# Optimization experiments

Measured on AMD Instinct MI355X. Metric: run time of the kernel, lower is better.

Reference implementation:

```python
import jax, jax.numpy as jnp
import numpy as np

DIM = 512
H = 8
HD = DIM // H
MAX_DIST = 128
TABLE = (2 * MAX_DIST + 1) ** 2
LAMBDA_INIT = 0.8


def setup_inputs() -> dict:
    key = jax.random.key(0)
    ks = jax.random.split(key, 20)
    B, Nq, Nkv = 4, 1024, 1024
    inp = {
        "x_q": jax.random.normal(ks[0], (B, Nq, DIM), jnp.float32),
        "x_kv": jax.random.normal(ks[1], (B, Nkv, DIM), jnp.float32),
        "coords_q": jax.random.randint(ks[2], (B, Nq, 2), 0, 256, jnp.int32),
        "coords_k": jax.random.randint(ks[3], (B, Nkv, 2), 0, 256, jnp.int32),
        "alpha_map": jax.random.uniform(ks[4], (B, Nq, 1), jnp.float32),
        "Wq": jax.random.normal(ks[5], (DIM, DIM), jnp.float32) * 0.02,
        "bq": jnp.zeros((DIM,), jnp.float32),
        "Wk": jax.random.normal(ks[6], (DIM, DIM), jnp.float32) * 0.02,
        "bk": jnp.zeros((DIM,), jnp.float32),
        "Wv": jax.random.normal(ks[7], (DIM, DIM), jnp.float32) * 0.02,
        "bv": jnp.zeros((DIM,), jnp.float32),
        "lambda_q1": jax.random.normal(ks[8], (H // 2, HD), jnp.float32) * 0.1,
        "lambda_k1": jax.random.normal(ks[9], (H // 2, HD), jnp.float32) * 0.1,
        "lambda_q2": jax.random.normal(ks[10], (H // 2, HD), jnp.float32) * 0.1,
        "lambda_k2": jax.random.normal(ks[11], (H // 2, HD), jnp.float32) * 0.1,
        "rpe_table": jax.random.normal(ks[12], (TABLE, H), jnp.float32) * 0.02,
        "Wp": jax.random.normal(ks[13], (DIM, DIM), jnp.float32) * 0.02,
        "bp": jnp.zeros((DIM,), jnp.float32),
    }
    return inp


def reference(x_q, x_kv, coords_q, coords_k, alpha_map,
              Wq, bq, Wk, bk, Wv, bv,
              lambda_q1, lambda_k1, lambda_q2, lambda_k2,
              rpe_table, Wp, bp):
    B, Nq, C = x_q.shape
    Nkv = x_kv.shape[1]
    n_half = H // 2
    scale = HD ** -0.5

    # projections -> [B, H, N, HD]
    q = (x_q @ Wq.T + bq).reshape(B, Nq, H, HD).transpose(0, 2, 1, 3)
    k = (x_kv @ Wk.T + bk).reshape(B, Nkv, H, HD).transpose(0, 2, 1, 3)
    v = (x_kv @ Wv.T + bv).reshape(B, Nkv, H, HD).transpose(0, 2, 1, 3)

    # sparse relative position bias: gather per-pair from table
    rel = coords_q[:, :, None, :] - coords_k[:, None, :, :] + MAX_DIST  # [B,Nq,Nkv,2]
    rel = jnp.clip(rel, 0, 2 * MAX_DIST)
    idx = rel[..., 0] * (2 * MAX_DIST + 1) + rel[..., 1]  # [B,Nq,Nkv]
    bias = rpe_table[idx].transpose(0, 3, 1, 2)  # [B,H,Nq,Nkv]

    scores = jnp.einsum('bhqd,bhkd->bhqk', q, k) * scale + bias
    probs = jax.nn.softmax(scores, axis=-1)
    x_std = jnp.einsum('bhqk,bhkd->bhqd', probs, v)

    lam1 = jnp.exp(jnp.sum(lambda_q1 * lambda_k1, axis=-1))  # [n_half]
    lam2 = jnp.exp(jnp.sum(lambda_q2 * lambda_k2, axis=-1))
    lam = (lam1 - lam2 + LAMBDA_INIT)[None, :, None, None]

    attn_diff = probs[:, :n_half] - lam * probs[:, n_half:]
    x_diff = jnp.einsum('bhqk,bhkd->bhqd', attn_diff, v[:, :n_half])

    alpha = alpha_map[:, None]  # [B,1,Nq,1]
    x1 = x_std[:, :n_half] + alpha * x_diff
    x = jnp.concatenate([x1, x_std[:, n_half:]], axis=1)  # [B,H,Nq,HD]
    x = x.transpose(0, 2, 1, 3).reshape(B, Nq, C)
    return x @ Wp.T + bp
```

## Files before the change

### kernel.cpp

```cpp
#include <hip/hip_runtime.h>
#include <cstddef>
#include <cstdint>

#define DIM   512
#define NSEQ  1024
#define NB    4
#define LOG2E 1.44269504f

typedef unsigned short u16;
typedef short bf16x8 __attribute__((ext_vector_type(8)));
typedef _Float16 half8v __attribute__((ext_vector_type(8)));
typedef float f32x4  __attribute__((ext_vector_type(4)));

#define MFMA(a, b, c)  __builtin_amdgcn_mfma_f32_16x16x32_bf16(a, b, c, 0, 0, 0)
#define MFMAH(a, b, c) __builtin_amdgcn_mfma_f32_16x16x32_f16(a, b, c, 0, 0, 0)

__device__ inline void split2(float x, u16& h, u16& l) {
  unsigned u = __float_as_uint(x);
  unsigned hb = (u + 0x7fffu + ((u >> 16) & 1u)) >> 16;
  float fh = __uint_as_float(hb << 16);
  float r = x - fh;
  unsigned v = __float_as_uint(r);
  unsigned lb = (v + 0x7fffu + ((v >> 16) & 1u)) >> 16;
  h = (u16)hb; l = (u16)lb;
}

__device__ inline uint2 pack4(const u16 a[4]) {
  return make_uint2((unsigned)a[0] | ((unsigned)a[1] << 16),
                    (unsigned)a[2] | ((unsigned)a[3] << 16));
}

__device__ inline u16 f2h(float x) {
  _Float16 h = (_Float16)x;
  u16 r; __builtin_memcpy(&r, &h, 2);
  return r;
}
__device__ inline float h2f(u16 b) {
  _Float16 h; __builtin_memcpy(&h, &b, 2);
  return (float)h;
}
__device__ inline unsigned pkh2(float a, float b) {
  return (unsigned)f2h(a) | ((unsigned)f2h(b) << 16);
}

__device__ inline void split_body(const float* __restrict__ in,
                                  u16* __restrict__ out, int e4) {
  const int e = e4 * 4;
  const int m = e >> 9, c = e & 511;
  const float4 v = *(const float4*)(in + e);
  u16 h[4], l[4];
  split2(v.x, h[0], l[0]); split2(v.y, h[1], l[1]);
  split2(v.z, h[2], l[2]); split2(v.w, h[3], l[3]);
  u16* o = out + (size_t)m * 1024 + c;
  *(uint2*)o = pack4(h);
  *(uint2*)(o + 512) = pack4(l);
}

#define GLDS(g, l)                                                        \
  __builtin_amdgcn_global_load_lds(                                       \
      (const __attribute__((address_space(1))) void*)(g),                 \
      (__attribute__((address_space(3))) void*)(l), 16, 0, 0)

__global__ __launch_bounds__(256) void prep(
    const float* __restrict__ wq, const float* __restrict__ wk,
    const float* __restrict__ wv, const float* __restrict__ wp,
    const float* __restrict__ xq, const float* __restrict__ xkv,
    const int* __restrict__ cq, const int* __restrict__ ck,
    const float* __restrict__ rpe,
    u16* __restrict__ w2, u16* __restrict__ xq2, u16* __restrict__ xkv2,
    u16* __restrict__ biasT) {
  __shared__ u16 Ts[8 * 16 * 64];
  const int id = blockIdx.x;
  const int t = threadIdx.x;
  if (id < 1024) {
    const int y = id >> 8;
    const float* src = (y == 0) ? wq : (y == 1) ? wk : (y == 2) ? wv : wp;
    split_body(src, w2 + (size_t)y * 524288, (id & 255) * 256 + t);
  } else if (id < 5120) {
    const int e = id - 1024;
    const int y = e >> 11;
    split_body(y ? xkv : xq, y ? xkv2 : xq2, (e & 2047) * 256 + t);
  } else {
    const int e = id - 5120;
    const int q0 = (e & 15) * 64, k0 = ((e >> 4) & 63) * 16, b = e >> 10;
    const int qn = t & 63, kb = t >> 6;
    const int2 cqv = ((const int2*)cq)[b * NSEQ + q0 + qn];
#pragma unroll
    for (int j = 0; j < 4; ++j) {
      const int k = kb * 4 + j;
      const int2 ckv = ((const int2*)ck)[b * NSEQ + k0 + k];
      const int r0 = min(max(cqv.x - ckv.x + 128, 0), 256);
      const int r1 = min(max(cqv.y - ckv.y + 128, 0), 256);
      const float* rp = rpe + (size_t)(r0 * 257 + r1) * 8;
      const float4 f0 = *(const float4*)rp;
      const float4 f1 = *(const float4*)(rp + 4);
      u16* dst = Ts + k * 64 + qn;
      dst[0 * 1024] = f2h(f0.x * LOG2E); dst[1 * 1024] = f2h(f0.y * LOG2E);
      dst[2 * 1024] = f2h(f0.z * LOG2E); dst[3 * 1024] = f2h(f0.w * LOG2E);
      dst[4 * 1024] = f2h(f1.x * LOG2E); dst[5 * 1024] = f2h(f1.y * LOG2E);
      dst[6 * 1024] = f2h(f1.z * LOG2E); dst[7 * 1024] = f2h(f1.w * LOG2E);
    }
    __syncthreads();
#pragma unroll
    for (int i = 0; i < 4; ++i) {
      const int e2 = i * 256 + t;
      const int row = e2 >> 3, c8 = e2 & 7;
      const int hh = row >> 4, k = row & 15;
      const uint4 v = *(const uint4*)(Ts + row * 64 + c8 * 8);
      *(uint4*)(biasT + ((size_t)(b * 8 + hh) * 1024 + k0 + k) * 1024 +
                q0 + c8 * 8) = v;
    }
  }
}

template <int OUT_MODE>
__device__ __forceinline__ void gemm_db(
    u16 (*__restrict__ As)[8192], u16 (*__restrict__ Bs)[8192],
    const u16* __restrict__ A2, const u16* __restrict__ B2,
    const float* __restrict__ bias, void* __restrict__ outp,
    float scale, int m0, int n0) {
  const int tid = threadIdx.x;
  const int lane = tid & 63, w = tid >> 6;
  const int wm = (w & 1) * 64, wn = (w >> 1) * 64;
  const int lr8 = lane >> 3;
  const int scc = (lane & 7) ^ lr8;
  const int colA = ((scc & 3) * 8) + ((scc >> 2) * 512);

  const int fr = lane & 15, kq = lane >> 4, fx = fr & 7;
  int aoh[4], aol[4], boh[4], bol[4];
#pragma unroll
  for (int i = 0; i < 4; ++i) {
    const int ra = (wm + i * 16 + fr) * 64;
    aoh[i] = ra + ((kq ^ fx)) * 8;
    aol[i] = ra + (((4 + kq) ^ fx)) * 8;
    const int rb = (wn + i * 16 + fr) * 64;
    boh[i] = rb + ((kq ^ fx)) * 8;
    bol[i] = rb + (((4 + kq) ^ fx)) * 8;
  }

  auto stage = [&](int it, int p) {
    const int k0 = it * 32;
#pragma unroll
    for (int i = 0; i < 4; ++i) {
      const int rA = m0 + w * 32 + i * 8 + lr8;
      GLDS(A2 + (size_t)rA * 1024 + colA + k0,
           (char*)As[p] + (w * 32 + i * 8) * 128);
      const int rB = n0 + w * 32 + i * 8 + lr8;
      GLDS(B2 + (size_t)rB * 1024 + colA + k0,
           (char*)Bs[p] + (w * 32 + i * 8) * 128);
    }
  };

  f32x4 acc[4][4] = {};
  stage(0, 0);
  for (int it = 0; it < 16; ++it) {
    const int p = it & 1;
    __syncthreads();
    if (it + 1 < 16) stage(it + 1, p ^ 1);
    const u16* Ab = As[p];
    const u16* Bb = Bs[p];
    bf16x8 ah[4], al[4], bh[4], bl[4];
#pragma unroll
    for (int i = 0; i < 4; ++i) {
      ah[i] = *(const bf16x8*)(Ab + aoh[i]);
      al[i] = *(const bf16x8*)(Ab + aol[i]);
      bh[i] = *(const bf16x8*)(Bb + boh[i]);
      bl[i] = *(const bf16x8*)(Bb + bol[i]);
    }
#pragma unroll
    for (int i = 0; i < 4; ++i)
#pragma unroll
      for (int j = 0; j < 4; ++j) {
        acc[i][j] = MFMA(al[i], bh[j], acc[i][j]);
        acc[i][j] = MFMA(ah[i], bl[j], acc[i][j]);
        acc[i][j] = MFMA(ah[i], bh[j], acc[i][j]);
      }
  }

  const int er = (lane >> 4) * 4, ec = lane & 15;
#pragma unroll
  for (int i = 0; i < 4; ++i)
#pragma unroll
    for (int j = 0; j < 4; ++j) {
      const int row = m0 + wm + i * 16 + er;
      const int col = n0 + wn + j * 16 + ec;
      const float bv = bias[col];
      if (OUT_MODE == 4) {
        u16 hf[4];
#pragma unroll
        for (int r = 0; r < 4; ++r) hf[r] = f2h((acc[i][j][r] + bv) * scale);
        const int bb = row >> 10, kk = row & 1023;
        *(uint2*)((u16*)outp + ((size_t)(bb * 512 + col)) * 1024 + kk) =
            pack4(hf);
      } else {
#pragma unroll
        for (int r = 0; r < 4; ++r) {
          const float v = (acc[i][j][r] + bv) * scale;
          if (OUT_MODE == 3)
            ((u16*)outp)[(size_t)(row + r) * 512 + col] = f2h(v);
          else
            ((float*)outp)[(size_t)(row + r) * 512 + col] = v;
        }
      }
    }
}

__global__ __launch_bounds__(256, 2) void gemm_qkv(
    const u16* __restrict__ xq2, const u16* __restrict__ xkv2,
    const u16* __restrict__ w2, const float* __restrict__ bq,
    const float* __restrict__ bk, const float* __restrict__ bv,
    u16* __restrict__ q2f, u16* __restrict__ k2f, u16* __restrict__ vtf) {
  __shared__ __align__(16) u16 As[2][8192], Bs[2][8192];
  const int z = blockIdx.z;
  const int m0 = blockIdx.x * 128, n0 = blockIdx.y * 128;
  if (z == 0)
    gemm_db<3>(As, Bs, xq2, w2, bq, q2f, 0.125f * LOG2E, m0, n0);
  else if (z == 1)
    gemm_db<3>(As, Bs, xkv2, w2 + 524288, bk, k2f, 1.0f, m0, n0);
  else
    gemm_db<4>(As, Bs, xkv2, w2 + 2 * 524288, bv, vtf, 1.0f, m0, n0);
}

__global__ __launch_bounds__(256, 2) void gemm_out(
    const u16* __restrict__ xa2, const u16* __restrict__ w2p,
    const float* __restrict__ bp, float* __restrict__ out) {
  __shared__ __align__(16) u16 As[2][8192], Bs[2][8192];
  gemm_db<0>(As, Bs, xa2, w2p, bp, out, 1.0f,
             blockIdx.x * 128, blockIdx.y * 128);
}

__global__ __launch_bounds__(512) void attn_f16(
    const u16* __restrict__ q2f, const u16* __restrict__ k2f,
    const u16* __restrict__ vtf, const float* __restrict__ amap,
    const float* __restrict__ lq1, const float* __restrict__ lk1,
    const float* __restrict__ lq2, const float* __restrict__ lk2,
    const u16* __restrict__ biasT, u16* __restrict__ xo) {
  __shared__ __align__(16) u16 KsL[2][2][4096];
  __shared__ __align__(16) u16 VtL[2][2][4096];
  __shared__ float2 mls[2][2][2][16];
  __shared__ float l2s[32];
  __shared__ float lam_s;

  const int tid = threadIdx.x;
  const int lane = tid & 63, w = tid >> 6;
  const int kg = w >> 2, h = (w >> 1) & 1, qs = w & 1;
  const int wl = w & 3;
  const int hp = blockIdx.y, b = blockIdx.z;
  const int q0 = blockIdx.x * 32;
  const int head = hp + 4 * h;
  const int lq = lane & 15, lg = lane >> 4;
  const int q = qs * 16 + lq;
  const size_t qrow = (size_t)(b * NSEQ + q0 + q);

  if (tid < 64) {
    float p1 = lq1[hp * 64 + tid] * lk1[hp * 64 + tid];
    float p2 = lq2[hp * 64 + tid] * lk2[hp * 64 + tid];
#pragma unroll
    for (int m = 32; m >= 1; m >>= 1) {
      p1 += __shfl_xor(p1, m, 64);
      p2 += __shfl_xor(p2, m, 64);
    }
    if (tid == 0) lam_s = __expf(p1) - __expf(p2) + 0.8f;
  }

  const float alpha = amap[qrow];

  half8v Qf[2];
#pragma unroll
  for (int ks = 0; ks < 2; ++ks)
    Qf[ks] = *(const half8v*)(q2f + qrow * 512 + head * 64 + ks * 32 + lg * 8);

  f32x4 Ya[4] = {};
  f32x4 Yb[4] = {};
  float m_run = -1e30f, l_run = 0.0f;

  const int lr = lane >> 3;
  const int lc = (lane & 7) ^ lr;
  const int cw = wl * 2;

  auto stage = [&](int it, int p) {
    const int kbase = kg * 512 + it * 32;
#pragma unroll
    for (int i = 0; i < 2; ++i) {
      const int c = cw + i;
      const int row = c * 8 + lr;
      const int sh = row >> 5, k = row & 31;
      const u16* src = k2f + (size_t)(b * NSEQ + kbase + k) * 512 +
                       (hp + 4 * sh) * 64 + lc * 8;
      GLDS(src, (char*)KsL[kg][p] + c * 1024);
    }
#pragma unroll
    for (int i = 0; i < 2; ++i) {
      const int c = cw + i;
      const int d = c * 8 + lr;
      const int hv = lc >> 2, kc = lc & 3;
      const u16* src = vtf + (size_t)(b * 512 + (hp + 4 * hv) * 64 + d) * 1024 +
                       kbase + kc * 8;
      GLDS(src, (char*)VtL[kg][p] + c * 1024);
    }
  };

  const u16* bT = biasT + ((size_t)(b * 8 + head) << 20) + q0 + q;

  stage(0, 0);

  for (int it = 0; it < 16; ++it) {
    const int p = it & 1;
    __syncthreads();
    if (it + 1 < 16) stage(it + 1, p ^ 1);

    u16 rb[8];
    {
      const u16* bt = bT + (size_t)(kg * 512 + it * 32) * 1024;
#pragma unroll
      for (int kt = 0; kt < 2; ++kt)
#pragma unroll
        for (int r = 0; r < 4; ++r)
          rb[kt * 4 + r] = bt[(size_t)(kt * 16 + lg * 4 + r) * 1024];
    }

    const u16* Kb = KsL[kg][p];
    f32x4 st[2] = {};
#pragma unroll
    for (int kt = 0; kt < 2; ++kt) {
      const int krow = kt * 16 + lq;
      const int rx = krow & 7;
#pragma unroll
      for (int ks = 0; ks < 2; ++ks) {
        const int phys = (ks * 4 + lg) ^ rx;
        const half8v kf = *(const half8v*)(Kb + (h * 32 + krow) * 64 + phys * 8);
        st[kt] = MFMAH(kf, Qf[ks], st[kt]);
      }
    }

    float sv[2][4];
    float mx = -1e30f;
#pragma unroll
    for (int kt = 0; kt < 2; ++kt)
#pragma unroll
      for (int r = 0; r < 4; ++r) {
        const float s = st[kt][r] + h2f(rb[kt * 4 + r]);
        sv[kt][r] = s;
        mx = fmaxf(mx, s);
      }
    mx = fmaxf(mx, __shfl_xor(mx, 16, 64));
    mx = fmaxf(mx, __shfl_xor(mx, 32, 64));
    const float mnew = fmaxf(m_run, mx);
    const float a = exp2f(m_run - mnew);
    m_run = mnew;
    float pr[2][4], ps = 0.0f;
#pragma unroll
    for (int kt = 0; kt < 2; ++kt)
#pragma unroll
      for (int r = 0; r < 4; ++r) {
        pr[kt][r] = exp2f(sv[kt][r] - mnew);
        ps += pr[kt][r];
      }
    ps += __shfl_xor(ps, 16, 64);
    ps += __shfl_xor(ps, 32, 64);
    l_run = l_run * a + ps;
#pragma unroll
    for (int dt = 0; dt < 4; ++dt) Ya[dt] *= a;
    if (h == 1) {
#pragma unroll
      for (int dt = 0; dt < 4; ++dt) Yb[dt] *= a;
    }

    const unsigned a0 = pkh2(pr[0][0], pr[0][1]);
    const unsigned a1 = pkh2(pr[0][2], pr[0][3]);
    const unsigned b0 = pkh2(pr[1][0], pr[1][1]);
    const unsigned b1 = pkh2(pr[1][2], pr[1][3]);
    const int srcA = lq + ((lg & 1) << 5);
    const unsigned A0 = __shfl((int)a0, srcA),      A1 = __shfl((int)a1, srcA);
    const unsigned B0 = __shfl((int)b0, srcA),      B1 = __shfl((int)b1, srcA);
    const unsigned C0 = __shfl((int)a0, srcA + 16), C1 = __shfl((int)a1, srcA + 16);
    const unsigned D0 = __shfl((int)b0, srcA + 16), D1 = __shfl((int)b1, srcA + 16);
    const bool t2 = lg >= 2;
    const uint4 Pu = make_uint4(t2 ? B0 : A0, t2 ? B1 : A1,
                                t2 ? D0 : C0, t2 ? D1 : C1);
    half8v pb;
    __builtin_memcpy(&pb, &Pu, 16);

    const u16* Vb = VtL[kg][p];
    if (h == 0) {
#pragma unroll
      for (int dt = 0; dt < 4; ++dt) {
        const int d = dt * 16 + lq;
        const half8v v1 = *(const half8v*)(Vb + d * 64 + ((lg ^ (d & 7))) * 8);
        Ya[dt] = MFMAH(v1, pb, Ya[dt]);
      }
    } else {
#pragma unroll
      for (int dt = 0; dt < 4; ++dt) {
        const int d = dt * 16 + lq;
        const int dx = d & 7;
        const half8v v1 = *(const half8v*)(Vb + d * 64 + ((lg ^ dx)) * 8);
        Yb[dt] = MFMAH(v1, pb, Yb[dt]);
        const half8v v2 = *(const half8v*)(Vb + d * 64 + (((4 + lg) ^ dx)) * 8);
        Ya[dt] = MFMAH(v2, pb, Ya[dt]);
      }
    }
  }

  float* mY = (float*)KsL;
  float* mB = (float*)VtL;
  __syncthreads();
  if (lane < 16) mls[kg][h][qs][lane] = make_float2(m_run, l_run);
  if (kg == 1) {
#pragma unroll
    for (int dt = 0; dt < 4; ++dt)
#pragma unroll
      for (int r = 0; r < 4; ++r)
        mY[((h * 2 + qs) * 64 + lane) * 16 + dt * 4 + r] = Ya[dt][r];
    if (h == 1) {
#pragma unroll
      for (int dt = 0; dt < 4; ++dt)
#pragma unroll
        for (int r = 0; r < 4; ++r)
          mB[(qs * 64 + lane) * 16 + dt * 4 + r] = Yb[dt][r];
    }
  }
  __syncthreads();
  float l_tot = l_run;
  if (kg == 0) {
    const float2 o = mls[1][h][qs][lq];
    const float mm = fmaxf(m_run, o.x);
    const float s0 = exp2f(m_run - mm);
    const float s1 = exp2f(o.x - mm);
    l_tot = l_run * s0 + o.y * s1;
    const float* sY = mY + ((h * 2 + qs) * 64 + lane) * 16;
#pragma unroll
    for (int dt = 0; dt < 4; ++dt)
#pragma unroll
      for (int r = 0; r < 4; ++r)
        Ya[dt][r] = Ya[dt][r] * s0 + sY[dt * 4 + r] * s1;
    if (h == 1) {
      const float* sB = mB + (qs * 64 + lane) * 16;
#pragma unroll
      for (int dt = 0; dt < 4; ++dt)
#pragma unroll
        for (int r = 0; r < 4; ++r)
          Yb[dt][r] = Yb[dt][r] * s0 + sB[dt * 4 + r] * s1;
    }
  }

  __syncthreads();
  float* y2x = (float*)KsL;
  if (kg == 0 && h == 1) {
    if (lane < 16) l2s[qs * 16 + lane] = l_tot;
#pragma unroll
    for (int dt = 0; dt < 4; ++dt)
#pragma unroll
      for (int r = 0; r < 4; ++r)
        y2x[(qs * 64 + lane) * 16 + dt * 4 + r] = Yb[dt][r];
  }
  __syncthreads();
  if (kg == 0 && h == 1) {
    const float inv2 = 1.0f / l_tot;
#pragma unroll
    for (int dt = 0; dt < 4; ++dt) {
      u16 hh[4], ll[4];
#pragma unroll
      for (int r = 0; r < 4; ++r) split2(Ya[dt][r] * inv2, hh[r], ll[r]);
      u16* o = xo + qrow * 1024 + (hp + 4) * 64 + dt * 16 + lg * 4;
      *(uint2*)o = pack4(hh);
      *(uint2*)(o + 512) = pack4(ll);
    }
  } else if (kg == 0 && h == 0) {
    const float inv1 = 1.0f / l_tot;
    const float inv2 = 1.0f / l2s[qs * 16 + lq];
    const float c1 = (1.0f + alpha) * inv1;
    const float c2 = alpha * lam_s * inv2;
#pragma unroll
    for (int dt = 0; dt < 4; ++dt) {
      u16 hh[4], ll[4];
#pragma unroll
      for (int r = 0; r < 4; ++r) {
        const float y2 = y2x[(qs * 64 + lane) * 16 + dt * 4 + r];
        split2(c1 * Ya[dt][r] - c2 * y2, hh[r], ll[r]);
      }
      u16* o = xo + qrow * 1024 + hp * 64 + dt * 16 + lg * 4;
      *(uint2*)o = pack4(hh);
      *(uint2*)(o + 512) = pack4(ll);
    }
  }
}

extern "C" void kernel_launch(void* const* d_in, const int* in_sizes, int n_in,
                              void* d_out, int out_size, void* d_ws, size_t ws_size,
                              hipStream_t stream) {
  const float* x_q   = (const float*)d_in[0];
  const float* x_kv  = (const float*)d_in[1];
  const int*   c_q   = (const int*)d_in[2];
  const int*   c_k   = (const int*)d_in[3];
  const float* alpha = (const float*)d_in[4];
  const float* Wq    = (const float*)d_in[5];
  const float* bq    = (const float*)d_in[6];
  const float* Wk    = (const float*)d_in[7];
  const float* bk    = (const float*)d_in[8];
  const float* Wv    = (const float*)d_in[9];
  const float* bv    = (const float*)d_in[10];
  const float* lq1   = (const float*)d_in[11];
  const float* lk1   = (const float*)d_in[12];
  const float* lq2   = (const float*)d_in[13];
  const float* lk2   = (const float*)d_in[14];
  const float* rpe   = (const float*)d_in[15];
  const float* Wp    = (const float*)d_in[16];
  const float* bp    = (const float*)d_in[17];

  u16* w2    = (u16*)d_ws;
  u16* xq2   = (u16*)((char*)d_ws + (4u << 20));
  u16* q2f   = (u16*)((char*)d_ws + (12u << 20));
  u16* k2f   = (u16*)((char*)d_ws + (16u << 20));
  u16* vtf   = (u16*)((char*)d_ws + (20u << 20));
  u16* xa    = xq2;
  u16* biasT = (u16*)((char*)d_ws + (28u << 20));
  u16* xkv2  = (u16*)d_out;

  prep<<<9216, 256, 0, stream>>>(Wq, Wk, Wv, Wp, x_q, x_kv, c_q, c_k, rpe,
                                 w2, xq2, xkv2, biasT);
  gemm_qkv<<<dim3(32, 4, 3), 256, 0, stream>>>(xq2, xkv2, w2, bq, bk, bv,
                                               q2f, k2f, vtf);
  attn_f16<<<dim3(32, 4, NB), 512, 0, stream>>>(
      q2f, k2f, vtf, alpha, lq1, lk1, lq2, lk2, biasT, xa);
  gemm_out<<<dim3(32, 4), 256, 0, stream>>>(xa, w2 + 3 * 524288, bp,
                                            (float*)d_out);
}
```

Baseline: 210.4 us.

## Co-schedule RPE bias gather with QKV GEMM and retile output projection

The relative-position bias gather moves out of the prep kernel and into the QKV GEMM launch as extra blocks, so the memory-bound gather can overlap with the compute-bound projection GEMM. The GEMM shared memory is reused as the transpose staging buffer. The output projection becomes a dedicated 128x64-tile kernel with a 64-wide K step and single buffering. That doubles its block count and targets three blocks per CU, at the cost of losing double-buffered prefetch.

```diff
diff --git a/kernel.cpp b/kernel.cpp
--- a/kernel.cpp
+++ b/kernel.cpp
@@ -61,27 +61,134 @@
       (const __attribute__((address_space(1))) void*)(g),                 \
       (__attribute__((address_space(3))) void*)(l), 16, 0, 0)
 
-__global__ __launch_bounds__(256) void prep(
+__global__ __launch_bounds__(256) void prep_split(
     const float* __restrict__ wq, const float* __restrict__ wk,
     const float* __restrict__ wv, const float* __restrict__ wp,
     const float* __restrict__ xq, const float* __restrict__ xkv,
-    const int* __restrict__ cq, const int* __restrict__ ck,
-    const float* __restrict__ rpe,
-    u16* __restrict__ w2, u16* __restrict__ xq2, u16* __restrict__ xkv2,
-    u16* __restrict__ biasT) {
-  __shared__ u16 Ts[8 * 16 * 64];
+    u16* __restrict__ w2, u16* __restrict__ xq2, u16* __restrict__ xkv2) {
   const int id = blockIdx.x;
   const int t = threadIdx.x;
   if (id < 1024) {
     const int y = id >> 8;
     const float* src = (y == 0) ? wq : (y == 1) ? wk : (y == 2) ? wv : wp;
     split_body(src, w2 + (size_t)y * 524288, (id & 255) * 256 + t);
-  } else if (id < 5120) {
+  } else {
     const int e = id - 1024;
     const int y = e >> 11;
     split_body(y ? xkv : xq, y ? xkv2 : xq2, (e & 2047) * 256 + t);
+  }
+}
+
+template <int OUT_MODE>
+__device__ __forceinline__ void gemm_db(
+    u16 (*__restrict__ As)[8192], u16 (*__restrict__ Bs)[8192],
+    const u16* __restrict__ A2, const u16* __restrict__ B2,
+    const float* __restrict__ bias, void* __restrict__ outp,
+    float scale, int m0, int n0) {
+  const int tid = threadIdx.x;
+  const int lane = tid & 63, w = tid >> 6;
+  const int wm = (w & 1) * 64, wn = (w >> 1) * 64;
+  const int lr8 = lane >> 3;
+  const int scc = (lane & 7) ^ lr8;
+  const int colA = ((scc & 3) * 8) + ((scc >> 2) * 512);
+
+  const int fr = lane & 15, kq = lane >> 4, fx = fr & 7;
+  int aoh[4], aol[4], boh[4], bol[4];
+#pragma unroll
+  for (int i = 0; i < 4; ++i) {
+    const int ra = (wm + i * 16 + fr) * 64;
+    aoh[i] = ra + ((kq ^ fx)) * 8;
+    aol[i] = ra + (((4 + kq) ^ fx)) * 8;
+    const int rb = (wn + i * 16 + fr) * 64;
+    boh[i] = rb + ((kq ^ fx)) * 8;
+    bol[i] = rb + (((4 + kq) ^ fx)) * 8;
+  }
+
+  auto stage = [&](int it, int p) {
+    const int k0 = it * 32;
+#pragma unroll
+    for (int i = 0; i < 4; ++i) {
+      const int rA = m0 + w * 32 + i * 8 + lr8;
+      GLDS(A2 + (size_t)rA * 1024 + colA + k0,
+           (char*)As[p] + (w * 32 + i * 8) * 128);
+      const int rB = n0 + w * 32 + i * 8 + lr8;
+      GLDS(B2 + (size_t)rB * 1024 + colA + k0,
+           (char*)Bs[p] + (w * 32 + i * 8) * 128);
+    }
+  };
+
+  f32x4 acc[4][4] = {};
+  stage(0, 0);
+  for (int it = 0; it < 16; ++it) {
+    const int p = it & 1;
+    __syncthreads();
+    if (it + 1 < 16) stage(it + 1, p ^ 1);
+    const u16* Ab = As[p];
+    const u16* Bb = Bs[p];
+    bf16x8 ah[4], al[4], bh[4], bl[4];
+#pragma unroll
+    for (int i = 0; i < 4; ++i) {
+      ah[i] = *(const bf16x8*)(Ab + aoh[i]);
+      al[i] = *(const bf16x8*)(Ab + aol[i]);
+      bh[i] = *(const bf16x8*)(Bb + boh[i]);
+      bl[i] = *(const bf16x8*)(Bb + bol[i]);
+    }
+#pragma unroll
+    for (int i = 0; i < 4; ++i)
+#pragma unroll
+      for (int j = 0; j < 4; ++j) {
+        acc[i][j] = MFMA(al[i], bh[j], acc[i][j]);
+        acc[i][j] = MFMA(ah[i], bl[j], acc[i][j]);
+        acc[i][j] = MFMA(ah[i], bh[j], acc[i][j]);
+      }
+  }
+
+  const int er = (lane >> 4) * 4, ec = lane & 15;
+#pragma unroll
+  for (int i = 0; i < 4; ++i)
+#pragma unroll
+    for (int j = 0; j < 4; ++j) {
+      const int row = m0 + wm + i * 16 + er;
+      const int col = n0 + wn + j * 16 + ec;
+      const float bv = bias[col];
+      if (OUT_MODE == 4) {
+        u16 hf[4];
+#pragma unroll
+        for (int r = 0; r < 4; ++r) hf[r] = f2h((acc[i][j][r] + bv) * scale);
+        const int bb = row >> 10, kk = row & 1023;
+        *(uint2*)((u16*)outp + ((size_t)(bb * 512 + col)) * 1024 + kk) =
+            pack4(hf);
+      } else {
+#pragma unroll
+        for (int r = 0; r < 4; ++r)
+          ((u16*)outp)[(size_t)(row + r) * 512 + col] =
+              f2h((acc[i][j][r] + bv) * scale);
+      }
+    }
+}
+
+__global__ __launch_bounds__(256) void qkv_rpe(
+    const u16* __restrict__ xq2, const u16* __restrict__ xkv2,
+    const u16* __restrict__ w2, const float* __restrict__ bq,
+    const float* __restrict__ bk, const float* __restrict__ bv,
+    u16* __restrict__ q2f, u16* __restrict__ k2f, u16* __restrict__ vtf,
+    const int* __restrict__ cq, const int* __restrict__ ck,
+    const float* __restrict__ rpe, u16* __restrict__ biasT) {
+  __shared__ __align__(16) u16 As[2][8192], Bs[2][8192];
+  const int id = blockIdx.x;
+  const int t = threadIdx.x;
+  if (id < 384) {
+    const int z = id >> 7, rem = id & 127;
+    const int m0 = (rem & 31) * 128, n0 = (rem >> 5) * 128;
+    if (z == 0)
+      gemm_db<3>(As, Bs, xq2, w2, bq, q2f, 0.125f * LOG2E, m0, n0);
+    else if (z == 1)
+      gemm_db<3>(As, Bs, xkv2, w2 + 524288, bk, k2f, 1.0f, m0, n0);
+    else
+      gemm_db<4>(As, Bs, xkv2, w2 + 2 * 524288, bv, vtf, 1.0f, m0, n0);
   } else {
-    const int e = id - 5120;
+    u16* Ts = (u16*)As;
+    const int e = id - 384;
     const int q0 = (e & 15) * 64, k0 = ((e >> 4) & 63) * 16, b = e >> 10;
     const int qn = t & 63, kb = t >> 6;
     const int2 cqv = ((const int2*)cq)[b * NSEQ + q0 + qn];
@@ -113,120 +220,84 @@
   }
 }
 
-template <int OUT_MODE>
-__device__ __forceinline__ void gemm_db(
-    u16 (*__restrict__ As)[8192], u16 (*__restrict__ Bs)[8192],
+__global__ __launch_bounds__(256, 3) void gemm_out(
     const u16* __restrict__ A2, const u16* __restrict__ B2,
-    const float* __restrict__ bias, void* __restrict__ outp,
-    float scale, int m0, int n0) {
+    const float* __restrict__ bias, float* __restrict__ out) {
+  __shared__ __align__(16) u16 Ah[8192], Al[8192], Bh[4096], Bl[4096];
+  const int m0 = blockIdx.x * 128, n0 = blockIdx.y * 64;
   const int tid = threadIdx.x;
   const int lane = tid & 63, w = tid >> 6;
-  const int wm = (w & 1) * 64, wn = (w >> 1) * 64;
-  const int lr8 = lane >> 3;
-  const int scc = (lane & 7) ^ lr8;
-  const int colA = ((scc & 3) * 8) + ((scc >> 2) * 512);
+  const int wm = (w & 1) * 64, wn = (w >> 1) * 32;
+  const int lr = lane >> 3;
+  const int scc = (lane & 7) ^ lr;
+
+  const u16* gA = A2 + (size_t)(m0 + w * 32 + lr) * 1024 + scc * 8;
+  const u16* gB = B2 + (size_t)(n0 + w * 16 + lr) * 1024 + scc * 8;
+  char* lAh = (char*)Ah + w * 4096;  char* lAl = (char*)Al + w * 4096;
+  char* lBh = (char*)Bh + w * 2048;  char* lBl = (char*)Bl + w * 2048;
 
   const int fr = lane & 15, kq = lane >> 4, fx = fr & 7;
-  int aoh[4], aol[4], boh[4], bol[4];
-#pragma unroll
-  for (int i = 0; i < 4; ++i) {
-    const int ra = (wm + i * 16 + fr) * 64;
-    aoh[i] = ra + ((kq ^ fx)) * 8;
-    aol[i] = ra + (((4 + kq) ^ fx)) * 8;
-    const int rb = (wn + i * 16 + fr) * 64;
-    boh[i] = rb + ((kq ^ fx)) * 8;
-    bol[i] = rb + (((4 + kq) ^ fx)) * 8;
-  }
-
-  auto stage = [&](int it, int p) {
-    const int k0 = it * 32;
+  int aoff[2][4], boff[2][2];
+#pragma unroll
+  for (int s = 0; s < 2; ++s) {
+#pragma unroll
+    for (int i = 0; i < 4; ++i)
+      aoff[s][i] = (wm + i * 16 + fr) * 64 + (((s * 4 + kq) ^ fx)) * 8;
+#pragma unroll
+    for (int j = 0; j < 2; ++j)
+      boff[s][j] = (wn + j * 16 + fr) * 64 + (((s * 4 + kq) ^ fx)) * 8;
+  }
+
+  f32x4 acc[4][2] = {};
+  for (int k0 = 0; k0 < 512; k0 += 64) {
+    __syncthreads();
 #pragma unroll
     for (int i = 0; i < 4; ++i) {
-      const int rA = m0 + w * 32 + i * 8 + lr8;
-      GLDS(A2 + (size_t)rA * 1024 + colA + k0,
-           (char*)As[p] + (w * 32 + i * 8) * 128);
-      const int rB = n0 + w * 32 + i * 8 + lr8;
-      GLDS(B2 + (size_t)rB * 1024 + colA + k0,
-           (char*)Bs[p] + (w * 32 + i * 8) * 128);
-    }
-  };
-
-  f32x4 acc[4][4] = {};
-  stage(0, 0);
-  for (int it = 0; it < 16; ++it) {
-    const int p = it & 1;
+      GLDS(gA + (size_t)i * 8192 + k0, lAh + i * 1024);
+      GLDS(gA + (size_t)i * 8192 + 512 + k0, lAl + i * 1024);
+    }
+#pragma unroll
+    for (int i = 0; i < 2; ++i) {
+      GLDS(gB + (size_t)i * 8192 + k0, lBh + i * 1024);
+      GLDS(gB + (size_t)i * 8192 + 512 + k0, lBl + i * 1024);
+    }
     __syncthreads();
-    if (it + 1 < 16) stage(it + 1, p ^ 1);
-    const u16* Ab = As[p];
-    const u16* Bb = Bs[p];
-    bf16x8 ah[4], al[4], bh[4], bl[4];
-#pragma unroll
-    for (int i = 0; i < 4; ++i) {
-      ah[i] = *(const bf16x8*)(Ab + aoh[i]);
-      al[i] = *(const bf16x8*)(Ab + aol[i]);
-      bh[i] = *(const bf16x8*)(Bb + boh[i]);
-      bl[i] = *(const bf16x8*)(Bb + bol[i]);
-    }
-#pragma unroll
-    for (int i = 0; i < 4; ++i)
-#pragma unroll
-      for (int j = 0; j < 4; ++j) {
-        acc[i][j] = MFMA(al[i], bh[j], acc[i][j]);
-        acc[i][j] = MFMA(ah[i], bl[j], acc[i][j]);
-        acc[i][j] = MFMA(ah[i], bh[j], acc[i][j]);
-      }
+#pragma unroll
+    for (int s = 0; s < 2; ++s) {
+      bf16x8 ah[4], al[4], bh[2], bl[2];
+#pragma unroll
+      for (int i = 0; i < 4; ++i) {
+        ah[i] = *(const bf16x8*)(Ah + aoff[s][i]);
+        al[i] = *(const bf16x8*)(Al + aoff[s][i]);
+      }
+#pragma unroll
+      for (int j = 0; j < 2; ++j) {
+        bh[j] = *(const bf16x8*)(Bh + boff[s][j]);
+        bl[j] = *(const bf16x8*)(Bl + boff[s][j]);
+      }
+#pragma unroll
+      for (int i = 0; i < 4; ++i)
+#pragma unroll
+        for (int j = 0; j < 2; ++j) {
+          acc[i][j] = MFMA(al[i], bh[j], acc[i][j]);
+          acc[i][j] = MFMA(ah[i], bl[j], acc[i][j]);
+          acc[i][j] = MFMA(ah[i], bh[j], acc[i][j]);
+        }
+    }
   }
 
   const int er = (lane >> 4) * 4, ec = lane & 15;
 #pragma unroll
   for (int i = 0; i < 4; ++i)
 #pragma unroll
-    for (int j = 0; j < 4; ++j) {
+    for (int j = 0; j < 2; ++j) {
       const int row = m0 + wm + i * 16 + er;
       const int col = n0 + wn + j * 16 + ec;
       const float bv = bias[col];
-      if (OUT_MODE == 4) {
-        u16 hf[4];
-#pragma unroll
-        for (int r = 0; r < 4; ++r) hf[r] = f2h((acc[i][j][r] + bv) * scale);
-        const int bb = row >> 10, kk = row & 1023;
-        *(uint2*)((u16*)outp + ((size_t)(bb * 512 + col)) * 1024 + kk) =
-            pack4(hf);
-      } else {
-#pragma unroll
-        for (int r = 0; r < 4; ++r) {
-          const float v = (acc[i][j][r] + bv) * scale;
-          if (OUT_MODE == 3)
-            ((u16*)outp)[(size_t)(row + r) * 512 + col] = f2h(v);
-          else
-            ((float*)outp)[(size_t)(row + r) * 512 + col] = v;
-        }
-      }
-    }
-}
-
-__global__ __launch_bounds__(256, 2) void gemm_qkv(
-    const u16* __restrict__ xq2, const u16* __restrict__ xkv2,
-    const u16* __restrict__ w2, const float* __restrict__ bq,
-    const float* __restrict__ bk, const float* __restrict__ bv,
-    u16* __restrict__ q2f, u16* __restrict__ k2f, u16* __restrict__ vtf) {
-  __shared__ __align__(16) u16 As[2][8192], Bs[2][8192];
-  const int z = blockIdx.z;
-  const int m0 = blockIdx.x * 128, n0 = blockIdx.y * 128;
-  if (z == 0)
-    gemm_db<3>(As, Bs, xq2, w2, bq, q2f, 0.125f * LOG2E, m0, n0);
-  else if (z == 1)
-    gemm_db<3>(As, Bs, xkv2, w2 + 524288, bk, k2f, 1.0f, m0, n0);
-  else
-    gemm_db<4>(As, Bs, xkv2, w2 + 2 * 524288, bv, vtf, 1.0f, m0, n0);
-}
-
-__global__ __launch_bounds__(256, 2) void gemm_out(
-    const u16* __restrict__ xa2, const u16* __restrict__ w2p,
-    const float* __restrict__ bp, float* __restrict__ out) {
-  __shared__ __align__(16) u16 As[2][8192], Bs[2][8192];
-  gemm_db<0>(As, Bs, xa2, w2p, bp, out, 1.0f,
-             blockIdx.x * 128, blockIdx.y * 128);
+#pragma unroll
+      for (int r = 0; r < 4; ++r)
+        out[(size_t)(row + r) * 512 + col] = acc[i][j][r] + bv;
+    }
 }
 
 __global__ __launch_bounds__(512) void attn_f16(
@@ -517,12 +588,12 @@
   u16* biasT = (u16*)((char*)d_ws + (28u << 20));
   u16* xkv2  = (u16*)d_out;
 
-  prep<<<9216, 256, 0, stream>>>(Wq, Wk, Wv, Wp, x_q, x_kv, c_q, c_k, rpe,
-                                 w2, xq2, xkv2, biasT);
-  gemm_qkv<<<dim3(32, 4, 3), 256, 0, stream>>>(xq2, xkv2, w2, bq, bk, bv,
-                                               q2f, k2f, vtf);
+  prep_split<<<5120, 256, 0, stream>>>(Wq, Wk, Wv, Wp, x_q, x_kv,
+                                       w2, xq2, xkv2);
+  qkv_rpe<<<4480, 256, 0, stream>>>(xq2, xkv2, w2, bq, bk, bv,
+                                    q2f, k2f, vtf, c_q, c_k, rpe, biasT);
   attn_f16<<<dim3(32, 4, NB), 512, 0, stream>>>(
       q2f, k2f, vtf, alpha, lq1, lk1, lq2, lk2, biasT, xa);
-  gemm_out<<<dim3(32, 4), 256, 0, stream>>>(xa, w2 + 3 * 524288, bp,
+  gemm_out<<<dim3(32, 8), 256, 0, stream>>>(xa, w2 + 3 * 524288, bp,
                                             (float*)d_out);
 }
```

Result: faster. 202.8 us (-3.6%).
